# Kernel optimization log

Measured on AMD Instinct MI355X. Metric: run time of the kernel, lower is better.

The kernel has to match this reference:

```python
import jax, jax.numpy as jnp
import numpy as np

B = 65536       # number of segments (molecules/graphs) = max(batch_indices[0]) + 1
N = 1048576     # nodes per eye
IN_NF, R_OUT, C_OUT = 64, 128, 128
BRAIN_IN, BRAIN_H, BRAIN_OUT = 256, 256, 128


def setup_inputs() -> dict:
    key = jax.random.key(0)
    ks = jax.random.split(key, 16)
    f = jax.random.normal
    s_in = 1.0 / np.sqrt(IN_NF)
    s_r = 1.0 / np.sqrt(R_OUT)
    s_b = 1.0 / np.sqrt(BRAIN_IN)
    s_h = 1.0 / np.sqrt(BRAIN_H)
    return {
        "x0": f(ks[0], (N, IN_NF), jnp.float32),
        "x1": f(ks[1], (N, IN_NF), jnp.float32),
        "idx0": jax.random.randint(ks[2], (N,), 0, B, dtype=jnp.int32),
        "idx1": jax.random.randint(ks[3], (N,), 0, B, dtype=jnp.int32),
        "Wr0": f(ks[4], (IN_NF, R_OUT), jnp.float32) * s_in,
        "br0": jnp.zeros((R_OUT,), jnp.float32),
        "Wc0": f(ks[5], (R_OUT, C_OUT), jnp.float32) * s_r,
        "bc0": jnp.zeros((C_OUT,), jnp.float32),
        "Wr1": f(ks[6], (IN_NF, R_OUT), jnp.float32) * s_in,
        "br1": jnp.zeros((R_OUT,), jnp.float32),
        "Wc1": f(ks[7], (R_OUT, C_OUT), jnp.float32) * s_r,
        "bc1": jnp.zeros((C_OUT,), jnp.float32),
        "Wb1": f(ks[8], (BRAIN_IN, BRAIN_H), jnp.float32) * s_b,
        "bb1": jnp.zeros((BRAIN_H,), jnp.float32),
        "Wb2": f(ks[9], (BRAIN_H, BRAIN_OUT), jnp.float32) * s_h,
        "bb2": jnp.zeros((BRAIN_OUT,), jnp.float32),
    }


def _eye(x, idx, Wr, br, Wc, bc):
    # linear + relu per node: [N, r_out]
    h = jax.nn.relu(x @ Wr + br)
    # scatter-mean over segments -> [B, r_out]; empty segments get 0 (matches
    # torch_scatter mean and the original zero-padding up to maxlen)
    s = jax.ops.segment_sum(h, idx, num_segments=B)
    cnt = jax.ops.segment_sum(jnp.ones((h.shape[0],), h.dtype), idx, num_segments=B)
    mean = s / jnp.maximum(cnt, 1.0)[:, None]
    # per-graph linear + relu -> [B, c_out]
    return jax.nn.relu(mean @ Wc + bc)


def reference(x0, x1, idx0, idx1, Wr0, br0, Wc0, bc0, Wr1, br1, Wc1, bc1, Wb1, bb1, Wb2, bb2):
    e0 = _eye(x0, idx0, Wr0, br0, Wc0, bc0)   # [B, 128]
    e1 = _eye(x1, idx1, Wr1, br1, Wc1, bc1)   # [B, 128]
    z = jnp.concatenate([e0, e1], axis=1)      # [B, 256]
    h = jax.nn.relu(z @ Wb1 + bb1)             # [B, 256]
    return h @ Wb2 + bb2                       # [B, 128]
```

## Files before the change

### kernel.cpp

```cpp
#include <hip/hip_runtime.h>
#include <hip/hip_bf16.h>

#define B_SEG 65536
#define N_NODES 1048576

typedef _Float16 f16;
typedef __attribute__((ext_vector_type(8))) _Float16 f16x8;
typedef __attribute__((ext_vector_type(2))) __fp16 fp16x2;
typedef __attribute__((ext_vector_type(4))) float f32x4;
typedef unsigned short u16;

union F16x8 { f16x8 v; fp16x2 h2[4]; };

#define MFMA16(a, b, acc) __builtin_amdgcn_mfma_f32_16x16x32_f16((a), (b), (acc), 0, 0, 0)

__global__ __launch_bounds__(256) void histo_part(const int* __restrict__ idx0,
        const int* __restrict__ idx1, int* __restrict__ cnt0, int* __restrict__ cnt1,
        u16* __restrict__ rankp0, u16* __restrict__ rankp1) {
    int part  = blockIdx.x & 7;
    int chunk = blockIdx.x >> 3;
    u16* r0 = rankp0 + (size_t)part * N_NODES;
    u16* r1 = rankp1 + (size_t)part * N_NODES;
    int base4 = chunk * (N_NODES / 256 / 4);
    for (int g = base4 + threadIdx.x; g < base4 + N_NODES / 256 / 4; g += 256) {
        int4 s0 = ((const int4*)idx0)[g];
        int i = g * 4;
        if ((s0.x >> 13) == part) { int p = atomicAdd(&cnt0[s0.x], 1); r0[i]     = (u16)p; }
        if ((s0.y >> 13) == part) { int p = atomicAdd(&cnt0[s0.y], 1); r0[i + 1] = (u16)p; }
        if ((s0.z >> 13) == part) { int p = atomicAdd(&cnt0[s0.z], 1); r0[i + 2] = (u16)p; }
        if ((s0.w >> 13) == part) { int p = atomicAdd(&cnt0[s0.w], 1); r0[i + 3] = (u16)p; }
        int4 s1 = ((const int4*)idx1)[g];
        if ((s1.x >> 13) == part) { int p = atomicAdd(&cnt1[s1.x], 1); r1[i]     = (u16)p; }
        if ((s1.y >> 13) == part) { int p = atomicAdd(&cnt1[s1.y], 1); r1[i + 1] = (u16)p; }
        if ((s1.z >> 13) == part) { int p = atomicAdd(&cnt1[s1.z], 1); r1[i + 2] = (u16)p; }
        if ((s1.w >> 13) == part) { int p = atomicAdd(&cnt1[s1.w], 1); r1[i + 3] = (u16)p; }
    }
}

__global__ __launch_bounds__(256) void scan1(const int* __restrict__ cnt, int* __restrict__ bsum) {
    int b = blockIdx.x, t = threadIdx.x;
    int4 v = ((const int4*)cnt)[b * 256 + t];
    int s = v.x + v.y + v.z + v.w;
    for (int d = 1; d < 64; d <<= 1) s += __shfl_xor(s, d);
    __shared__ int ws4[4];
    if ((t & 63) == 0) ws4[t >> 6] = s;
    __syncthreads();
    if (t == 0) bsum[b] = ws4[0] + ws4[1] + ws4[2] + ws4[3];
}

__global__ __launch_bounds__(128) void scan2(int* __restrict__ bsum) {
    int t = threadIdx.x, lane = t & 63;
    int v = bsum[t];
    int s = v;
    for (int d = 1; d < 64; d <<= 1) { int u = __shfl_up(s, d); if (lane >= d) s += u; }
    bsum[t] = s - v;
}

__global__ __launch_bounds__(256) void scan3(const int* __restrict__ cnt, const int* __restrict__ bsum,
                                             int* __restrict__ off0, int* __restrict__ off1) {
    int b = blockIdx.x, t = threadIdx.x;
    int4 v = ((const int4*)cnt)[b * 256 + t];
    int local = v.x + v.y + v.z + v.w;
    int lane = t & 63, w = t >> 6;
    int s = local;
    for (int d = 1; d < 64; d <<= 1) { int u = __shfl_up(s, d); if (lane >= d) s += u; }
    __shared__ int wsum[4];
    if (lane == 63) wsum[w] = s;
    __syncthreads();
    int carry = bsum[b];
    for (int i = 0; i < w; ++i) carry += wsum[i];
    int ex = carry + s - local;
    int* off = (b < 64) ? off0 : off1;
    int gi = (b & 63) * 1024 + t * 4;
    off[gi] = ex; ex += v.x; off[gi + 1] = ex; ex += v.y; off[gi + 2] = ex; ex += v.z; off[gi + 3] = ex;
    if (b == 0 && t == 0) { off0[B_SEG] = N_NODES; off1[B_SEG] = N_NODES; }
}

__global__ __launch_bounds__(256) void fill_prep(const int* __restrict__ idx0,
        const int* __restrict__ idx1, const u16* __restrict__ rankp0, const u16* __restrict__ rankp1,
        const int* __restrict__ off0, const int* __restrict__ off1,
        int* __restrict__ ord0, int* __restrict__ ord1,
        const float* __restrict__ Wc0, const float* __restrict__ Wc1,
        const float* __restrict__ Wb1, const float* __restrict__ Wb2,
        f16* __restrict__ T0, f16* __restrict__ T1, f16* __restrict__ T2, f16* __restrict__ T3) {
    if (blockIdx.x < 2048) {
        int part  = blockIdx.x & 7;
        int chunk = blockIdx.x >> 3;
        const u16* r0 = rankp0 + (size_t)part * N_NODES;
        const u16* r1 = rankp1 + (size_t)part * N_NODES;
        int base4 = chunk * (N_NODES / 256 / 4);
        for (int g = base4 + threadIdx.x; g < base4 + N_NODES / 256 / 4; g += 256) {
            int4 s0 = ((const int4*)idx0)[g];
            ushort4 q0 = ((const ushort4*)r0)[g];
            int i = g * 4;
            if ((s0.x >> 13) == part) ord0[off0[s0.x] + q0.x] = i;
            if ((s0.y >> 13) == part) ord0[off0[s0.y] + q0.y] = i + 1;
            if ((s0.z >> 13) == part) ord0[off0[s0.z] + q0.z] = i + 2;
            if ((s0.w >> 13) == part) ord0[off0[s0.w] + q0.w] = i + 3;
            int4 s1 = ((const int4*)idx1)[g];
            ushort4 q1 = ((const ushort4*)r1)[g];
            if ((s1.x >> 13) == part) ord1[off1[s1.x] + q1.x] = i;
            if ((s1.y >> 13) == part) ord1[off1[s1.y] + q1.y] = i + 1;
            if ((s1.z >> 13) == part) ord1[off1[s1.z] + q1.z] = i + 2;
            if ((s1.w >> 13) == part) ord1[off1[s1.w] + q1.w] = i + 3;
        }
    } else {
        int b = blockIdx.x - 2048, t = threadIdx.x;
        if (b < 64)        { int i = b * 256 + t;         T0[i] = (f16)Wc0[(i & 127) * 128 + (i >> 7)]; }
        else if (b < 128)  { int i = (b - 64) * 256 + t;  T1[i] = (f16)Wc1[(i & 127) * 128 + (i >> 7)]; }
        else if (b < 384)  { int i = (b - 128) * 256 + t; T2[i] = (f16)Wb1[(i & 255) * 256 + (i >> 8)]; }
        else               { int i = (b - 384) * 256 + t; T3[i] = (f16)Wb2[(i & 255) * 128 + (i >> 8)]; }
    }
}

#define SEGS_PER_WAVE 8
__global__ __launch_bounds__(256, 3) void eye_means_mfma(
        const float* __restrict__ xA, const float* __restrict__ WrA, const float* __restrict__ brA,
        const int* __restrict__ offA, const int* __restrict__ ordA, f16* __restrict__ meansA,
        const float* __restrict__ xB, const float* __restrict__ WrB, const float* __restrict__ brB,
        const int* __restrict__ offB, const int* __restrict__ ordB, f16* __restrict__ meansB) {
    const float *x, *Wr, *br; const int *off, *ord; f16* means;
    if (blockIdx.y == 0) { x = xA; Wr = WrA; br = brA; off = offA; ord = ordA; means = meansA; }
    else                 { x = xB; Wr = WrB; br = brB; off = offB; ord = ordB; means = meansB; }

    int lane = threadIdx.x & 63;
    int wid  = blockIdx.x * 4 + (threadIdx.x >> 6);
    int c  = lane & 15;
    int kq = lane >> 4;

    f16x8 bfr[8][2];
    float rbias[8];
    #pragma unroll
    for (int g = 0; g < 8; ++g) {
        #pragma unroll
        for (int h = 0; h < 2; ++h)
            #pragma unroll
            for (int j = 0; j < 8; ++j)
                bfr[g][h][j] = (f16)Wr[(size_t)(h * 32 + kq * 8 + j) * 128 + g * 16 + c];
        rbias[g] = br[g * 16 + c];
    }

    int s_begin = wid * SEGS_PER_WAVE;
    int offv  = off[s_begin + ((lane <= 8) ? lane : 8)];
    int base0 = __shfl(offv, 0);
    int nxtv  = __shfl(offv, (lane < 8) ? (lane + 1) : 8);
    int szl   = nxtv - offv;

    int ov0 = ord[base0 + lane];
    int ov1 = ord[base0 + 64 + lane];
    int ov2 = ord[base0 + 128 + lane];

    auto node_at = [&](int off_rel, int sz, int r) -> int {
        int e  = off_rel + r;
        int e6 = e & 63;
        int n0 = __shfl(ov0, e6);
        int n1 = __shfl(ov1, e6);
        int n2 = __shfl(ov2, e6);
        int n  = (e < 64) ? n0 : (e < 128) ? n1 : n2;
        if (e >= 192) n = ord[base0 + e];
        return (r < sz) ? n : 0;
    };

    auto loadx = [&](int node, float4& v0, float4& v1, float4& v2, float4& v3) {
        const float* xp = &x[(size_t)node * 64 + kq * 8];
        v0 = *(const float4*)(xp);      v1 = *(const float4*)(xp + 4);
        v2 = *(const float4*)(xp + 32); v3 = *(const float4*)(xp + 36);
    };

    float sum[8];
    #pragma unroll
    for (int g = 0; g < 8; ++g) sum[g] = 0.f;

    float4 ca, cb, cc, cd;
    {
        int sz0 = __shfl(szl, 0);
        loadx(node_at(0, sz0, c), ca, cb, cc, cd);
    }

    #pragma unroll
    for (int s = 0; s < SEGS_PER_WAVE; ++s) {
        int off_rel   = __shfl(offv, s) - base0;
        int sz        = __shfl(szl, s);
        int nb        = (sz + 15) >> 4;
        int off_rel_n = (s < SEGS_PER_WAVE - 1) ? (__shfl(offv, s + 1) - base0) : 0;
        int sz_n      = (s < SEGS_PER_WAVE - 1) ? __shfl(szl, s + 1) : 0;
        size_t mb     = (size_t)(s_begin + s) * 128;

        if (nb == 0) {
            means[mb + (2 * kq + 0) * 16 + c] = (f16)0.f;
            means[mb + (2 * kq + 1) * 16 + c] = (f16)0.f;
            loadx(node_at(off_rel_n, sz_n, c), ca, cb, cc, cd);
            continue;
        }

        for (int b = 0; b < nb; ++b) {
            int nn = (b + 1 < nb) ? node_at(off_rel, sz, (b + 1) * 16 + c)
                                  : node_at(off_rel_n, sz_n, c);
            float4 pa, pb, pc, pd;
            loadx(nn, pa, pb, pc, pd);

            f16x8 A0 = {}, A1 = {};
            if (b * 16 + c < sz) {
                F16x8 u0, u1;
                u0.h2[0] = __builtin_amdgcn_cvt_pkrtz(ca.x, ca.y);
                u0.h2[1] = __builtin_amdgcn_cvt_pkrtz(ca.z, ca.w);
                u0.h2[2] = __builtin_amdgcn_cvt_pkrtz(cb.x, cb.y);
                u0.h2[3] = __builtin_amdgcn_cvt_pkrtz(cb.z, cb.w);
                u1.h2[0] = __builtin_amdgcn_cvt_pkrtz(cc.x, cc.y);
                u1.h2[1] = __builtin_amdgcn_cvt_pkrtz(cc.z, cc.w);
                u1.h2[2] = __builtin_amdgcn_cvt_pkrtz(cd.x, cd.y);
                u1.h2[3] = __builtin_amdgcn_cvt_pkrtz(cd.z, cd.w);
                A0 = u0.v; A1 = u1.v;
            }
            #pragma unroll
            for (int g = 0; g < 8; ++g) {
                f32x4 acc = {0.f, 0.f, 0.f, 0.f};
                acc = MFMA16(A0, bfr[g][0], acc);
                acc = MFMA16(A1, bfr[g][1], acc);
                #pragma unroll
                for (int r = 0; r < 4; ++r)
                    sum[g] += fmaxf(acc[r] + rbias[g], 0.f);
            }
            ca = pa; cb = pb; cc = pc; cd = pd;
        }

        float padc = (float)(nb * 16 - sz);
        float inv  = 1.f / (float)sz;
        #pragma unroll
        for (int g = 0; g < 8; ++g) {
            float v = sum[g];
            v += __shfl_xor(v, 16);
            v += __shfl_xor(v, 32);
            v -= padc * fmaxf(rbias[g], 0.f);
            sum[g] = v * inv;
        }
        means[mb + (2 * kq + 0) * 16 + c] = (f16)sum[2 * kq + 0];
        means[mb + (2 * kq + 1) * 16 + c] = (f16)sum[2 * kq + 1];
        #pragma unroll
        for (int g = 0; g < 8; ++g) sum[g] = 0.f;
    }
}

template<int K, int RELU, int OUT16>
__global__ __launch_bounds__(256) void gemm16(
        const f16* __restrict__ A, const f16* __restrict__ BT,
        const float* __restrict__ bias, void* __restrict__ Cv, int ldc) {
    int lane = threadIdx.x & 63;
    int w = threadIdx.x >> 6;
    int c = lane & 15, kq = lane >> 4;
    int m0 = blockIdx.x * 128 + w * 32;
    int n0 = blockIdx.y * 128;

    f32x4 acc[2][8] = {};
    const f16* arow0 = A + (size_t)(m0 + c) * K + kq * 8;
    const f16* arow1 = arow0 + (size_t)16 * K;
    const f16* brow  = BT + (size_t)(n0 + c) * K + kq * 8;

    #pragma unroll 2
    for (int k0 = 0; k0 < K; k0 += 32) {
        f16x8 a0 = *(const f16x8*)(arow0 + k0);
        f16x8 a1 = *(const f16x8*)(arow1 + k0);
        #pragma unroll
        for (int g = 0; g < 8; ++g) {
            f16x8 bf = *(const f16x8*)(brow + (size_t)g * 16 * K + k0);
            acc[0][g] = MFMA16(a0, bf, acc[0][g]);
            acc[1][g] = MFMA16(a1, bf, acc[1][g]);
        }
    }

    #pragma unroll
    for (int g = 0; g < 8; ++g) {
        float bv = bias[n0 + g * 16 + c];
        #pragma unroll
        for (int ms = 0; ms < 2; ++ms) {
            #pragma unroll
            for (int r = 0; r < 4; ++r) {
                float v = acc[ms][g][r] + bv;
                if (RELU) v = fmaxf(v, 0.f);
                size_t ci = (size_t)(m0 + ms * 16 + kq * 4 + r) * ldc + n0 + g * 16 + c;
                if (OUT16) ((f16*)Cv)[ci] = (f16)v;
                else       ((float*)Cv)[ci] = v;
            }
        }
    }
}

__global__ __launch_bounds__(256) void gemm_wc(
        const f16* __restrict__ M0, const f16* __restrict__ M1,
        const f16* __restrict__ T0, const f16* __restrict__ T1,
        const float* __restrict__ bc0, const float* __restrict__ bc1,
        f16* __restrict__ z) {
    int e = blockIdx.y;
    const f16* A  = e ? M1 : M0;
    const f16* BT = e ? T1 : T0;
    const float* bias = e ? bc1 : bc0;
    int lane = threadIdx.x & 63;
    int w = threadIdx.x >> 6;
    int c = lane & 15, kq = lane >> 4;
    int m0 = blockIdx.x * 128 + w * 32;

    f32x4 acc[2][8] = {};
    const f16* arow0 = A + (size_t)(m0 + c) * 128 + kq * 8;
    const f16* arow1 = arow0 + (size_t)16 * 128;
    const f16* brow  = BT + (size_t)c * 128 + kq * 8;

    #pragma unroll
    for (int k0 = 0; k0 < 128; k0 += 32) {
        f16x8 a0 = *(const f16x8*)(arow0 + k0);
        f16x8 a1 = *(const f16x8*)(arow1 + k0);
        #pragma unroll
        for (int g = 0; g < 8; ++g) {
            f16x8 bf = *(const f16x8*)(brow + (size_t)g * 16 * 128 + k0);
            acc[0][g] = MFMA16(a0, bf, acc[0][g]);
            acc[1][g] = MFMA16(a1, bf, acc[1][g]);
        }
    }

    #pragma unroll
    for (int g = 0; g < 8; ++g) {
        float bv = bias[g * 16 + c];
        #pragma unroll
        for (int ms = 0; ms < 2; ++ms) {
            #pragma unroll
            for (int r = 0; r < 4; ++r) {
                float v = fmaxf(acc[ms][g][r] + bv, 0.f);
                z[(size_t)(m0 + ms * 16 + kq * 4 + r) * 256 + e * 128 + g * 16 + c] = (f16)v;
            }
        }
    }
}

extern "C" void kernel_launch(void* const* d_in, const int* in_sizes, int n_in,
                              void* d_out, int out_size, void* d_ws, size_t ws_size,
                              hipStream_t stream) {
    const float* x0  = (const float*)d_in[0];
    const float* x1  = (const float*)d_in[1];
    const int*   idx0 = (const int*)d_in[2];
    const int*   idx1 = (const int*)d_in[3];
    const float* Wr0 = (const float*)d_in[4];
    const float* br0 = (const float*)d_in[5];
    const float* Wc0 = (const float*)d_in[6];
    const float* bc0 = (const float*)d_in[7];
    const float* Wr1 = (const float*)d_in[8];
    const float* br1 = (const float*)d_in[9];
    const float* Wc1 = (const float*)d_in[10];
    const float* bc1 = (const float*)d_in[11];
    const float* Wb1 = (const float*)d_in[12];
    const float* bb1 = (const float*)d_in[13];
    const float* Wb2 = (const float*)d_in[14];
    const float* bb2 = (const float*)d_in[15];
    float* out = (float*)d_out;

    char* w = (char*)d_ws;
    auto alloc = [&](size_t bytes) { void* p = (void*)w; w += (bytes + 255) & ~(size_t)255; return p; };
    int* cnt0 = (int*)alloc((size_t)B_SEG * 4);
    int* cnt1 = (int*)alloc((size_t)B_SEG * 4);
    int* off0 = (int*)alloc((size_t)(B_SEG + 1) * 4);
    int* off1 = (int*)alloc((size_t)(B_SEG + 1) * 4);
    int* ord0 = (int*)alloc((size_t)(N_NODES + 256) * 4);
    int* ord1 = (int*)alloc((size_t)(N_NODES + 256) * 4);
    u16* rankp0 = (u16*)alloc((size_t)8 * N_NODES * 2);
    u16* rankp1 = (u16*)alloc((size_t)8 * N_NODES * 2);
    int* bsum = (int*)alloc(128 * 4);
    f16* means0 = (f16*)alloc((size_t)B_SEG * 128 * 2);
    f16* means1 = (f16*)alloc((size_t)B_SEG * 128 * 2);
    f16* z      = (f16*)alloc((size_t)B_SEG * 256 * 2);
    f16* hb     = (f16*)alloc((size_t)B_SEG * 256 * 2);
    f16* T0     = (f16*)alloc((size_t)128 * 128 * 2);
    f16* T1     = (f16*)alloc((size_t)128 * 128 * 2);
    f16* T2     = (f16*)alloc((size_t)256 * 256 * 2);
    f16* T3     = (f16*)alloc((size_t)128 * 256 * 2);

    (void)hipMemsetAsync(cnt0, 0, 2 * (size_t)B_SEG * sizeof(int), stream);
    histo_part<<<2048, 256, 0, stream>>>(idx0, idx1, cnt0, cnt1, rankp0, rankp1);
    scan1<<<128, 256, 0, stream>>>(cnt0, bsum);
    scan2<<<1, 128, 0, stream>>>(bsum);
    scan3<<<128, 256, 0, stream>>>(cnt0, bsum, off0, off1);
    fill_prep<<<2048 + 512, 256, 0, stream>>>(idx0, idx1, rankp0, rankp1, off0, off1,
                                              ord0, ord1, Wc0, Wc1, Wb1, Wb2, T0, T1, T2, T3);

    eye_means_mfma<<<dim3(2048, 2), 256, 0, stream>>>(
        x0, Wr0, br0, off0, ord0, means0,
        x1, Wr1, br1, off1, ord1, means1);

    gemm_wc<<<dim3(512, 2), 256, 0, stream>>>(means0, means1, T0, T1, bc0, bc1, z);
    gemm16<256, 1, 1><<<dim3(512, 2), 256, 0, stream>>>(z,  T2, bb1, hb,  256);
    gemm16<256, 0, 0><<<dim3(512, 1), 256, 0, stream>>>(hb, T3, bb2, out, 128);
}
```

Measured before the change: 421.0 us.

## Pipeline gathered node loads through LDS with a flattened block work list

The per-segment nested loop in the eye kernel becomes a flat list of 16-node blocks across the wave's 8 segments. Each block's x rows are gathered with global_load_lds straight into a 3-slot per-wave LDS ring, keeping two blocks in flight ahead of compute. The aim is to hide gather latency better than the old single-register prefetch, at the cost of 48KB of LDS per block, which may lower occupancy. The ord padding is enlarged because the pipeline can read past the end of the list.

Measured after the change: 462.7 us. +9.9%, slower.

```diff
diff --git a/kernel.cpp b/kernel.cpp
--- a/kernel.cpp
+++ b/kernel.cpp
@@ -13,6 +13,10 @@
 union F16x8 { f16x8 v; fp16x2 h2[4]; };
 
 #define MFMA16(a, b, acc) __builtin_amdgcn_mfma_f32_16x16x32_f16((a), (b), (acc), 0, 0, 0)
+
+typedef __attribute__((address_space(1))) const void GV;
+typedef __attribute__((address_space(3))) void LV;
+#define GLOAD_LDS16(g, l) __builtin_amdgcn_global_load_lds((GV*)(g), (LV*)(l), 16, 0, 0)
 
 __global__ __launch_bounds__(256) void histo_part(const int* __restrict__ idx0,
         const int* __restrict__ idx1, int* __restrict__ cnt0, int* __restrict__ cnt1,
@@ -114,6 +118,7 @@
 }
 
 #define SEGS_PER_WAVE 8
+#define DEPTH 3
 __global__ __launch_bounds__(256, 3) void eye_means_mfma(
         const float* __restrict__ xA, const float* __restrict__ WrA, const float* __restrict__ brA,
         const int* __restrict__ offA, const int* __restrict__ ordA, f16* __restrict__ meansA,
@@ -123,10 +128,13 @@
     if (blockIdx.y == 0) { x = xA; Wr = WrA; br = brA; off = offA; ord = ordA; means = meansA; }
     else                 { x = xB; Wr = WrB; br = brB; off = offB; ord = ordB; means = meansB; }
 
+    __shared__ char ldsraw[4][DEPTH][4096];
     int lane = threadIdx.x & 63;
-    int wid  = blockIdx.x * 4 + (threadIdx.x >> 6);
+    int wv   = threadIdx.x >> 6;
+    int wid  = blockIdx.x * 4 + wv;
     int c  = lane & 15;
     int kq = lane >> 4;
+    char* myslots = &ldsraw[wv][0][0];
 
     f16x8 bfr[8][2];
     float rbias[8];
@@ -145,71 +153,87 @@
     int base0 = __shfl(offv, 0);
     int nxtv  = __shfl(offv, (lane < 8) ? (lane + 1) : 8);
     int szl   = nxtv - offv;
+    int nbl   = (szl + 15) >> 4;
 
     int ov0 = ord[base0 + lane];
     int ov1 = ord[base0 + 64 + lane];
     int ov2 = ord[base0 + 128 + lane];
 
-    auto node_at = [&](int off_rel, int sz, int r) -> int {
-        int e  = off_rel + r;
-        int e6 = e & 63;
+    int totalNB = 0;
+    #pragma unroll
+    for (int s = 0; s < 8; ++s) totalNB += __shfl(nbl, s);
+
+    auto pool_fetch = [&](int ei) -> int {
+        int e6 = ei & 63;
         int n0 = __shfl(ov0, e6);
         int n1 = __shfl(ov1, e6);
         int n2 = __shfl(ov2, e6);
-        int n  = (e < 64) ? n0 : (e < 128) ? n1 : n2;
-        if (e >= 192) n = ord[base0 + e];
-        return (r < sz) ? n : 0;
+        int n  = (ei < 64) ? n0 : (ei < 128) ? n1 : n2;
+        if (ei >= 192) n = ord[base0 + ei];
+        return n;
     };
 
-    auto loadx = [&](int node, float4& v0, float4& v1, float4& v2, float4& v3) {
-        const float* xp = &x[(size_t)node * 64 + kq * 8];
-        v0 = *(const float4*)(xp);      v1 = *(const float4*)(xp + 4);
-        v2 = *(const float4*)(xp + 32); v3 = *(const float4*)(xp + 36);
-    };
-
     float sum[8];
     #pragma unroll
     for (int g = 0; g < 8; ++g) sum[g] = 0.f;
-
-    float4 ca, cb, cc, cd;
-    {
-        int sz0 = __shfl(szl, 0);
-        loadx(node_at(0, sz0, c), ca, cb, cc, cd);
-    }
-
-    #pragma unroll
-    for (int s = 0; s < SEGS_PER_WAVE; ++s) {
-        int off_rel   = __shfl(offv, s) - base0;
-        int sz        = __shfl(szl, s);
-        int nb        = (sz + 15) >> 4;
-        int off_rel_n = (s < SEGS_PER_WAVE - 1) ? (__shfl(offv, s + 1) - base0) : 0;
-        int sz_n      = (s < SEGS_PER_WAVE - 1) ? __shfl(szl, s + 1) : 0;
-        size_t mb     = (size_t)(s_begin + s) * 128;
-
-        if (nb == 0) {
-            means[mb + (2 * kq + 0) * 16 + c] = (f16)0.f;
-            means[mb + (2 * kq + 1) * 16 + c] = (f16)0.f;
-            loadx(node_at(off_rel_n, sz_n, c), ca, cb, cc, cd);
-            continue;
-        }
-
-        for (int b = 0; b < nb; ++b) {
-            int nn = (b + 1 < nb) ? node_at(off_rel, sz, (b + 1) * 16 + c)
-                                  : node_at(off_rel_n, sz_n, c);
-            float4 pa, pb, pc, pd;
-            loadx(nn, pa, pb, pc, pd);
-
-            f16x8 A0 = {}, A1 = {};
-            if (b * 16 + c < sz) {
+    const f16x8 zf = {};
+
+    int e = 0;
+    while (e < totalNB) {
+        int chunk_n = totalNB - e;
+        if (chunk_n > 64) chunk_n = 64;
+
+        int bb = e + lane;
+        int cum = 0, s_of = 7, b_of = 0;
+        bool found = false;
+        #pragma unroll
+        for (int s = 0; s < 8; ++s) {
+            int nbs = __shfl(nbl, s);
+            if (!found && bb < cum + nbs) { s_of = s; b_of = bb - cum; found = true; }
+            cum += nbs;
+        }
+        int offs  = __shfl(offv, s_of) - base0;
+        int szs   = __shfl(szl, s_of);
+        int rs_t  = offs + b_of * 16;
+        int ren_t = offs + szs;
+        int sg_t  = s_of;
+
+        auto issue_item = [&](int el, int slot) {
+            int rs  = __shfl(rs_t,  el & 63);
+            int ren = __shfl(ren_t, el & 63);
+            int ei  = rs + c;
+            int n   = pool_fetch(ei);
+            int node = (ei < ren) ? n : 0;
+            const float* xp = &x[(size_t)node * 64 + kq * 8];
+            char* lb = myslots + slot * 4096;
+            GLOAD_LDS16(xp,      lb);
+            GLOAD_LDS16(xp + 4,  lb + 1024);
+            GLOAD_LDS16(xp + 32, lb + 2048);
+            GLOAD_LDS16(xp + 36, lb + 3072);
+        };
+
+        auto do_item = [&](int el, int slot) {
+            int rsX  = __shfl(rs_t,  el & 63);
+            int renX = __shfl(ren_t, el & 63);
+            asm volatile("s_waitcnt vmcnt(8)" ::: "memory");
+            __builtin_amdgcn_sched_barrier(0);
+            const float4* sp = (const float4*)(myslots + slot * 4096);
+            float4 va = sp[lane];
+            float4 vb = sp[64 + lane];
+            float4 vc = sp[128 + lane];
+            float4 vd = sp[192 + lane];
+            bool valid = (rsX + c < renX);
+            f16x8 A0 = zf, A1 = zf;
+            if (valid) {
                 F16x8 u0, u1;
-                u0.h2[0] = __builtin_amdgcn_cvt_pkrtz(ca.x, ca.y);
-                u0.h2[1] = __builtin_amdgcn_cvt_pkrtz(ca.z, ca.w);
-                u0.h2[2] = __builtin_amdgcn_cvt_pkrtz(cb.x, cb.y);
-                u0.h2[3] = __builtin_amdgcn_cvt_pkrtz(cb.z, cb.w);
-                u1.h2[0] = __builtin_amdgcn_cvt_pkrtz(cc.x, cc.y);
-                u1.h2[1] = __builtin_amdgcn_cvt_pkrtz(cc.z, cc.w);
-                u1.h2[2] = __builtin_amdgcn_cvt_pkrtz(cd.x, cd.y);
-                u1.h2[3] = __builtin_amdgcn_cvt_pkrtz(cd.z, cd.w);
+                u0.h2[0] = __builtin_amdgcn_cvt_pkrtz(va.x, va.y);
+                u0.h2[1] = __builtin_amdgcn_cvt_pkrtz(va.z, va.w);
+                u0.h2[2] = __builtin_amdgcn_cvt_pkrtz(vb.x, vb.y);
+                u0.h2[3] = __builtin_amdgcn_cvt_pkrtz(vb.z, vb.w);
+                u1.h2[0] = __builtin_amdgcn_cvt_pkrtz(vc.x, vc.y);
+                u1.h2[1] = __builtin_amdgcn_cvt_pkrtz(vc.z, vc.w);
+                u1.h2[2] = __builtin_amdgcn_cvt_pkrtz(vd.x, vd.y);
+                u1.h2[3] = __builtin_amdgcn_cvt_pkrtz(vd.z, vd.w);
                 A0 = u0.v; A1 = u1.v;
             }
             #pragma unroll
@@ -221,23 +245,50 @@
                 for (int r = 0; r < 4; ++r)
                     sum[g] += fmaxf(acc[r] + rbias[g], 0.f);
             }
-            ca = pa; cb = pb; cc = pc; cd = pd;
-        }
-
-        float padc = (float)(nb * 16 - sz);
-        float inv  = 1.f / (float)sz;
-        #pragma unroll
-        for (int g = 0; g < 8; ++g) {
-            float v = sum[g];
-            v += __shfl_xor(v, 16);
-            v += __shfl_xor(v, 32);
-            v -= padc * fmaxf(rbias[g], 0.f);
-            sum[g] = v * inv;
-        }
-        means[mb + (2 * kq + 0) * 16 + c] = (f16)sum[2 * kq + 0];
-        means[mb + (2 * kq + 1) * 16 + c] = (f16)sum[2 * kq + 1];
-        #pragma unroll
-        for (int g = 0; g < 8; ++g) sum[g] = 0.f;
+            if (renX - rsX <= 16) {
+                int sg  = __shfl(sg_t, el & 63);
+                int szS = __shfl(szl, sg);
+                int nbS = __shfl(nbl, sg);
+                float padc = (float)(nbS * 16 - szS);
+                float inv  = 1.f / (float)szS;
+                size_t mb  = (size_t)(s_begin + sg) * 128;
+                #pragma unroll
+                for (int g = 0; g < 8; ++g) {
+                    float v = sum[g];
+                    v += __shfl_xor(v, 16);
+                    v += __shfl_xor(v, 32);
+                    v -= padc * fmaxf(rbias[g], 0.f);
+                    sum[g] = v * inv;
+                }
+                means[mb + (2 * kq + 0) * 16 + c] = (f16)sum[2 * kq + 0];
+                means[mb + (2 * kq + 1) * 16 + c] = (f16)sum[2 * kq + 1];
+                #pragma unroll
+                for (int g = 0; g < 8; ++g) sum[g] = 0.f;
+            }
+        };
+
+        issue_item(0, 0);
+        issue_item(1, 1);
+        int sI = 2, sC = 0;
+        for (int el = 0; el < chunk_n; ++el) {
+            issue_item(el + 2, sI);
+            sI = (sI == DEPTH - 1) ? 0 : sI + 1;
+            do_item(el, sC);
+            sC = (sC == DEPTH - 1) ? 0 : sC + 1;
+        }
+        asm volatile("s_waitcnt vmcnt(0)" ::: "memory");
+        __builtin_amdgcn_sched_barrier(0);
+        e += chunk_n;
+    }
+
+    #pragma unroll
+    for (int s = 0; s < 8; ++s) {
+        int szS = __shfl(szl, s);
+        if (szS == 0) {
+            size_t mb = (size_t)(s_begin + s) * 128;
+            means[mb + (2 * kq + 0) * 16 + c] = (f16)0.f;
+            means[mb + (2 * kq + 1) * 16 + c] = (f16)0.f;
+        }
     }
 }
 
@@ -357,8 +408,8 @@
     int* cnt1 = (int*)alloc((size_t)B_SEG * 4);
     int* off0 = (int*)alloc((size_t)(B_SEG + 1) * 4);
     int* off1 = (int*)alloc((size_t)(B_SEG + 1) * 4);
-    int* ord0 = (int*)alloc((size_t)(N_NODES + 256) * 4);
-    int* ord1 = (int*)alloc((size_t)(N_NODES + 256) * 4);
+    int* ord0 = (int*)alloc((size_t)(N_NODES + 4096) * 4);
+    int* ord1 = (int*)alloc((size_t)(N_NODES + 4096) * 4);
     u16* rankp0 = (u16*)alloc((size_t)8 * N_NODES * 2);
     u16* rankp1 = (u16*)alloc((size_t)8 * N_NODES * 2);
     int* bsum = (int*)alloc(128 * 4);
```

## Stage gathered node rows into LDS via async global_load_lds double buffering

Applied to the files above, without the earlier changes.

Replaces the register-prefetched gather of x rows with direct global-to-LDS async loads (global_load_lds, 16 bytes per lane) into a per-wave double buffer. It uses a swizzled LDS layout and explicit vmcnt waits, so the next batch's gather overlaps the current batch's MFMA work. This frees the VGPRs that held prefetched rows and makes the gathered loads more coalesced (4 lanes per row). The cost is 32KB of LDS per block, which can lower occupancy, plus hand-placed waitcnt and scheduling barriers. The ord buffers are also padded further, likely to absorb the wider index reads.

Result: faster. 398.9 us (median of 2 runs) (-5.2%).

```diff
diff --git a/kernel.cpp b/kernel.cpp
--- a/kernel.cpp
+++ b/kernel.cpp
@@ -13,6 +13,10 @@
 union F16x8 { f16x8 v; fp16x2 h2[4]; };
 
 #define MFMA16(a, b, acc) __builtin_amdgcn_mfma_f32_16x16x32_f16((a), (b), (acc), 0, 0, 0)
+
+typedef __attribute__((address_space(1))) const void GV;
+typedef __attribute__((address_space(3))) void LV;
+#define GLOAD_LDS16(g, l) __builtin_amdgcn_global_load_lds((GV*)(g), (LV*)(l), 16, 0, 0)
 
 __global__ __launch_bounds__(256) void histo_part(const int* __restrict__ idx0,
         const int* __restrict__ idx1, int* __restrict__ cnt0, int* __restrict__ cnt1,
@@ -123,10 +127,13 @@
     if (blockIdx.y == 0) { x = xA; Wr = WrA; br = brA; off = offA; ord = ordA; means = meansA; }
     else                 { x = xB; Wr = WrB; br = brB; off = offB; ord = ordB; means = meansB; }
 
+    __shared__ char ldsraw[4][2][4096];
     int lane = threadIdx.x & 63;
-    int wid  = blockIdx.x * 4 + (threadIdx.x >> 6);
+    int wv   = threadIdx.x >> 6;
+    int wid  = blockIdx.x * 4 + wv;
     int c  = lane & 15;
     int kq = lane >> 4;
+    char* myslots = &ldsraw[wv][0][0];
 
     f16x8 bfr[8][2];
     float rbias[8];
@@ -161,21 +168,63 @@
         return (r < sz) ? n : 0;
     };
 
-    auto loadx = [&](int node, float4& v0, float4& v1, float4& v2, float4& v3) {
-        const float* xp = &x[(size_t)node * 64 + kq * 8];
-        v0 = *(const float4*)(xp);      v1 = *(const float4*)(xp + 4);
-        v2 = *(const float4*)(xp + 32); v3 = *(const float4*)(xp + 36);
+    int lrow = lane >> 2;
+    int lq   = lane & 3;
+    int lqg  = (lq + (lrow >> 1)) & 3;
+    auto issue_batch = [&](int off_rel2, int sz2, int b2, int slot) {
+        int node = node_at(off_rel2, sz2, b2 * 16 + lrow);
+        const float* gp = x + (size_t)node * 64 + lqg * 4;
+        char* lb = myslots + slot * 4096;
+        GLOAD_LDS16(gp,      lb);
+        GLOAD_LDS16(gp + 16, lb + 1024);
+        GLOAD_LDS16(gp + 32, lb + 2048);
+        GLOAD_LDS16(gp + 48, lb + 3072);
     };
 
     float sum[8];
     #pragma unroll
     for (int g = 0; g < 8; ++g) sum[g] = 0.f;
-
-    float4 ca, cb, cc, cd;
+    const f16x8 zf = {};
+
+    int h1o = (kq >> 1) * 1024 + c * 64;
+    int q1o = ((((kq & 1) * 2)     - (c >> 1)) & 3) * 16;
+    int q2o = ((((kq & 1) * 2 + 1) - (c >> 1)) & 3) * 16;
+
+    auto compute_batch = [&](int slot, int b2, int sz2) {
+        const char* lb = myslots + slot * 4096;
+        float4 va = *(const float4*)(lb + h1o + q1o);
+        float4 vb = *(const float4*)(lb + h1o + q2o);
+        float4 vc = *(const float4*)(lb + 2048 + h1o + q1o);
+        float4 vd = *(const float4*)(lb + 2048 + h1o + q2o);
+        f16x8 A0 = zf, A1 = zf;
+        if (b2 * 16 + c < sz2) {
+            F16x8 u0, u1;
+            u0.h2[0] = __builtin_amdgcn_cvt_pkrtz(va.x, va.y);
+            u0.h2[1] = __builtin_amdgcn_cvt_pkrtz(va.z, va.w);
+            u0.h2[2] = __builtin_amdgcn_cvt_pkrtz(vb.x, vb.y);
+            u0.h2[3] = __builtin_amdgcn_cvt_pkrtz(vb.z, vb.w);
+            u1.h2[0] = __builtin_amdgcn_cvt_pkrtz(vc.x, vc.y);
+            u1.h2[1] = __builtin_amdgcn_cvt_pkrtz(vc.z, vc.w);
+            u1.h2[2] = __builtin_amdgcn_cvt_pkrtz(vd.x, vd.y);
+            u1.h2[3] = __builtin_amdgcn_cvt_pkrtz(vd.z, vd.w);
+            A0 = u0.v; A1 = u1.v;
+        }
+        #pragma unroll
+        for (int g = 0; g < 8; ++g) {
+            f32x4 acc = {0.f, 0.f, 0.f, 0.f};
+            acc = MFMA16(A0, bfr[g][0], acc);
+            acc = MFMA16(A1, bfr[g][1], acc);
+            #pragma unroll
+            for (int r = 0; r < 4; ++r)
+                sum[g] += fmaxf(acc[r] + rbias[g], 0.f);
+        }
+    };
+
     {
         int sz0 = __shfl(szl, 0);
-        loadx(node_at(0, sz0, c), ca, cb, cc, cd);
-    }
+        issue_batch(0, sz0, 0, 0);
+    }
+    int cur = 0;
 
     #pragma unroll
     for (int s = 0; s < SEGS_PER_WAVE; ++s) {
@@ -189,39 +238,20 @@
         if (nb == 0) {
             means[mb + (2 * kq + 0) * 16 + c] = (f16)0.f;
             means[mb + (2 * kq + 1) * 16 + c] = (f16)0.f;
-            loadx(node_at(off_rel_n, sz_n, c), ca, cb, cc, cd);
+            asm volatile("s_waitcnt vmcnt(0)" ::: "memory");
+            __builtin_amdgcn_sched_barrier(0);
+            issue_batch(off_rel_n, sz_n, 0, cur);
             continue;
         }
 
         for (int b = 0; b < nb; ++b) {
-            int nn = (b + 1 < nb) ? node_at(off_rel, sz, (b + 1) * 16 + c)
-                                  : node_at(off_rel_n, sz_n, c);
-            float4 pa, pb, pc, pd;
-            loadx(nn, pa, pb, pc, pd);
-
-            f16x8 A0 = {}, A1 = {};
-            if (b * 16 + c < sz) {
-                F16x8 u0, u1;
-                u0.h2[0] = __builtin_amdgcn_cvt_pkrtz(ca.x, ca.y);
-                u0.h2[1] = __builtin_amdgcn_cvt_pkrtz(ca.z, ca.w);
-                u0.h2[2] = __builtin_amdgcn_cvt_pkrtz(cb.x, cb.y);
-                u0.h2[3] = __builtin_amdgcn_cvt_pkrtz(cb.z, cb.w);
-                u1.h2[0] = __builtin_amdgcn_cvt_pkrtz(cc.x, cc.y);
-                u1.h2[1] = __builtin_amdgcn_cvt_pkrtz(cc.z, cc.w);
-                u1.h2[2] = __builtin_amdgcn_cvt_pkrtz(cd.x, cd.y);
-                u1.h2[3] = __builtin_amdgcn_cvt_pkrtz(cd.z, cd.w);
-                A0 = u0.v; A1 = u1.v;
-            }
-            #pragma unroll
-            for (int g = 0; g < 8; ++g) {
-                f32x4 acc = {0.f, 0.f, 0.f, 0.f};
-                acc = MFMA16(A0, bfr[g][0], acc);
-                acc = MFMA16(A1, bfr[g][1], acc);
-                #pragma unroll
-                for (int r = 0; r < 4; ++r)
-                    sum[g] += fmaxf(acc[r] + rbias[g], 0.f);
-            }
-            ca = pa; cb = pb; cc = pc; cd = pd;
+            int nxt = cur ^ 1;
+            if (b + 1 < nb) issue_batch(off_rel, sz, b + 1, nxt);
+            else            issue_batch(off_rel_n, sz_n, 0, nxt);
+            asm volatile("s_waitcnt vmcnt(4)" ::: "memory");
+            __builtin_amdgcn_sched_barrier(0);
+            compute_batch(cur, b, sz);
+            cur = nxt;
         }
 
         float padc = (float)(nb * 16 - sz);
@@ -357,8 +387,8 @@
     int* cnt1 = (int*)alloc((size_t)B_SEG * 4);
     int* off0 = (int*)alloc((size_t)(B_SEG + 1) * 4);
     int* off1 = (int*)alloc((size_t)(B_SEG + 1) * 4);
-    int* ord0 = (int*)alloc((size_t)(N_NODES + 256) * 4);
-    int* ord1 = (int*)alloc((size_t)(N_NODES + 256) * 4);
+    int* ord0 = (int*)alloc((size_t)(N_NODES + 4096) * 4);
+    int* ord1 = (int*)alloc((size_t)(N_NODES + 4096) * 4);
     u16* rankp0 = (u16*)alloc((size_t)8 * N_NODES * 2);
     u16* rankp1 = (u16*)alloc((size_t)8 * N_NODES * 2);
     int* bsum = (int*)alloc(128 * 4);
```
